# Kernel optimization log

Hardware: AMD Instinct MI355X
Metric: run time of the kernel (lower is better)

## Reference

```python
import jax, jax.numpy as jnp
import numpy as np

N_NODES = 10000
N_EDGES = 160000
F = 128
NRB = 32


def setup_inputs() -> dict:
    key = jax.random.key(0)
    ks = jax.random.split(key, 20)
    inp = {
        "s": jax.random.normal(ks[0], (N_NODES, F), jnp.float32),
        "v": jax.random.normal(ks[1], (N_NODES, 3, F), jnp.float32),
        "radial_embeddings_1": jax.random.normal(ks[2], (N_EDGES, NRB), jnp.float32),
        "radial_embeddings_2": jax.random.normal(ks[3], (N_EDGES, NRB), jnp.float32),
        "radial_embeddings_3": jax.random.normal(ks[4], (N_EDGES, NRB), jnp.float32),
        "f_cut_1": jax.random.uniform(ks[5], (N_EDGES,), jnp.float32),
        "f_cut_2": jax.random.uniform(ks[6], (N_EDGES,), jnp.float32),
        "f_cut_3": jax.random.uniform(ks[7], (N_EDGES,), jnp.float32),
        "unit_vectors_1": jax.random.normal(ks[8], (N_EDGES, 3), jnp.float32),
        "unit_vectors_2": jax.random.normal(ks[9], (N_EDGES, 3), jnp.float32),
        "unit_vectors_3": jax.random.normal(ks[10], (N_EDGES, 3), jnp.float32),
        "edge_index": jax.random.randint(ks[11], (2, N_EDGES), 0, N_NODES, jnp.int64),
    }
    # parameters (Linear uses y = x @ W.T + b; we store transposed for x @ W)
    sc1 = 1.0 / np.sqrt(F)
    sc2 = 1.0 / np.sqrt(NRB)
    inp["W1"] = jax.random.uniform(ks[12], (F, F), jnp.float32, -sc1, sc1)
    inp["b1"] = jax.random.uniform(ks[13], (F,), jnp.float32, -sc1, sc1)
    inp["W2"] = jax.random.uniform(ks[14], (F, 8 * F), jnp.float32, -sc1, sc1)
    inp["b2"] = jax.random.uniform(ks[15], (8 * F,), jnp.float32, -sc1, sc1)
    inp["Wr"] = jax.random.uniform(ks[16], (NRB, 8 * F), jnp.float32, -sc2, sc2)
    inp["br"] = jax.random.uniform(ks[17], (8 * F,), jnp.float32, -sc2, sc2)
    return inp


def reference(s, v, radial_embeddings_1, radial_embeddings_2, radial_embeddings_3,
              f_cut_1, f_cut_2, f_cut_3,
              unit_vectors_1, unit_vectors_2, unit_vectors_3,
              edge_index, W1, b1, W2, b2, Wr, br):
    idx_i, idx_j = edge_index[0], edge_index[1]
    n_nodes = s.shape[0]
    nf = W1.shape[0]

    # phi = Linear(F,F) -> SiLU -> Linear(F,8F)   [N, 8F]
    phi = jax.nn.silu(s @ W1 + b1) @ W2 + b2

    # shared-weight radial filter over 3 branches  [E, 8F]
    W = ((radial_embeddings_1 @ Wr + br) * f_cut_1[:, None]
         + (radial_embeddings_2 @ Wr + br) * f_cut_2[:, None]
         + (radial_embeddings_3 @ Wr + br) * f_cut_3[:, None])

    x = phi[idx_j] * W                                    # [E, 8F]
    x_s, x_vv, x_vs1, x_vs2, x_vs3, x_vc1, x_vc2, x_vc3 = jnp.split(x, 8, axis=-1)

    ds = jax.ops.segment_sum(x_s, idx_i, num_segments=n_nodes)

    vj = v[idx_j]                                         # [E, 3, F]
    ex = lambda a: a[:, None, :]                          # [E,1,F] broadcast over xyz
    cr = lambda u: jnp.cross(vj, u[..., None], axis=1)    # [E, 3, F]

    x_v = (vj * ex(x_vv)
           + ex(x_vs1) * unit_vectors_1[..., None]
           + ex(x_vs2) * unit_vectors_2[..., None]
           + ex(x_vs3) * unit_vectors_3[..., None]
           + ex(x_vc1) * cr(unit_vectors_1)
           + ex(x_vc2) * cr(unit_vectors_2)
           + ex(x_vc3) * cr(unit_vectors_3))              # [E, 3, F]

    dv = jax.ops.segment_sum(x_v, idx_i, num_segments=n_nodes)
    return (s + ds, v + dv)
```

## Files before the change

### kernel.cpp

```cpp
#include <hip/hip_runtime.h>

#define N_NODES 10000
#define N_EDGES 160000
#define MAXT     19400
#define NSLOT    (MAXT * 16 + 16)
#define MSG_GRID 5000
#define PHI_BLOCKS 628
#define RC_BLOCKS 5000
#define PAD_BLOCKS 625

typedef __attribute__((ext_vector_type(8))) __bf16 bf16x8;
typedef __attribute__((ext_vector_type(8))) unsigned short u16x8;
typedef __attribute__((ext_vector_type(4))) float f32x4;

static __device__ __forceinline__ unsigned short f2bf(float x) {
    union { float f; unsigned u; } un;
    un.f = x;
    unsigned r = un.u + 0x7fffu + ((un.u >> 16) & 1u);
    return (unsigned short)(r >> 16);
}

static __device__ __forceinline__ float bf2f(unsigned short h) {
    union { unsigned u; float f; } un;
    un.u = ((unsigned)h) << 16;
    return un.f;
}

__global__ __launch_bounds__(256) void init_kernel(
    const float* __restrict__ s, const float* __restrict__ v,
    const int* __restrict__ eix,
    const float* __restrict__ W1, const float* __restrict__ W2,
    const float* __restrict__ Wr,
    float* __restrict__ out0, float* __restrict__ out1,
    unsigned short* __restrict__ vbf2, int* __restrict__ cnt,
    unsigned short* __restrict__ W1T, unsigned short* __restrict__ W2T,
    unsigned short* __restrict__ WrT)
{
    int tid = blockIdx.x * 256 + threadIdx.x;
    if (tid < N_NODES * 96)
        reinterpret_cast<float4*>(out1)[tid] = reinterpret_cast<const float4*>(v)[tid];
    if (tid < N_NODES * 32)
        reinterpret_cast<float4*>(out0)[tid] = reinterpret_cast<const float4*>(s)[tid];
    if (tid < N_NODES * 128) {
        int n = tid >> 7, f = tid & 127;
        ushort4 q;
        q.x = f2bf(v[(size_t)n * 384 + f]);
        q.y = f2bf(v[(size_t)n * 384 + 128 + f]);
        q.z = f2bf(v[(size_t)n * 384 + 256 + f]);
        q.w = 0;
        *reinterpret_cast<ushort4*>(vbf2 + (size_t)tid * 4) = q;
    }
    if (tid < 131072) {
        int n = tid >> 7, k = tid & 127;
        W2T[tid] = f2bf(W2[k * 1024 + n]);
    }
    if (tid < 16384) {
        int n = tid >> 7, k = tid & 127;
        W1T[tid] = f2bf(W1[k * 128 + n]);
    }
    if (tid < 32768) {
        int n = tid >> 5, k = tid & 31;
        WrT[tid] = f2bf(Wr[k * 1024 + n]);
    }
    if (tid < N_EDGES) atomicAdd(&cnt[eix[tid]], 1);
}

__global__ __launch_bounds__(256) void scan_phi_kernel(
    const int* __restrict__ cnt, int* __restrict__ cursor,
    int* __restrict__ nb, int* __restrict__ tile_node,
    int* __restrict__ ntiles,
    const float* __restrict__ s, const unsigned short* __restrict__ W1T,
    const float* __restrict__ b1, const unsigned short* __restrict__ W2T,
    const float* __restrict__ b2, unsigned short* __restrict__ phi2)
{
    __shared__ unsigned short h_lds[64][136];
    __shared__ int ws4[4];
    int bx = blockIdx.x;
    int t = threadIdx.x, lane = t & 63, w = t >> 6;

    if (bx == PHI_BLOCKS) {
        int n0 = t * 40;
        int sum = 0;
        for (int i = 0; i < 40; ++i) {
            int n = n0 + i;
            if (n < N_NODES) sum += (cnt[n] + 15) >> 4;
        }
        int x = sum;
        #pragma unroll
        for (int o = 1; o < 64; o <<= 1) {
            int y = __shfl_up(x, o);
            if (lane >= o) x += y;
        }
        if (lane == 63) ws4[w] = x;
        __syncthreads();
        if (t < 4) {
            int v = ws4[t];
            #pragma unroll
            for (int o = 1; o < 4; o <<= 1) {
                int y = __shfl_up(v, o);
                if (lane >= o) v += y;
            }
            ws4[t] = v;
        }
        __syncthreads();
        int wb = w ? ws4[w - 1] : 0;
        int run = wb + x - sum;
        for (int i = 0; i < 40; ++i) {
            int n = n0 + i;
            if (n >= N_NODES) break;
            int tc = (cnt[n] + 15) >> 4;
            nb[n] = run * 16;
            cursor[n] = run * 16;
            for (int k = 0; k < tc; ++k) tile_node[run + k] = n;
            run += tc;
        }
        if (t == 255) *ntiles = run;
        return;
    }

    int quad = lane >> 4, l16 = lane & 15;
    int m0 = (bx >> 2) * 64;
    int colg = bx & 3;

    int arow = m0 + w * 16 + l16;
    if (arow > N_NODES - 1) arow = N_NODES - 1;
    bf16x8 afr[4];
    #pragma unroll
    for (int ks = 0; ks < 4; ++ks) {
        const float* sp = s + (size_t)arow * 128 + ks * 32 + quad * 8;
        #pragma unroll
        for (int jj = 0; jj < 8; ++jj) afr[ks][jj] = (__bf16)sp[jj];
    }
    #pragma unroll
    for (int cg = 0; cg < 8; ++cg) {
        int col = cg * 16 + l16;
        f32x4 acc = {0.f, 0.f, 0.f, 0.f};
        #pragma unroll
        for (int ks = 0; ks < 4; ++ks) {
            bf16x8 bf = *reinterpret_cast<const bf16x8*>(W1T + (size_t)col * 128 + ks * 32 + quad * 8);
            acc = __builtin_amdgcn_mfma_f32_16x16x32_bf16(afr[ks], bf, acc, 0, 0, 0);
        }
        float bb = b1[col];
        #pragma unroll
        for (int r = 0; r < 4; ++r) {
            int row = w * 16 + quad * 4 + r;
            float val = acc[r] + bb;
            h_lds[row][col] = f2bf(val / (1.f + __expf(-val)));
        }
    }
    __syncthreads();

    bf16x8 a2[4][4];
    #pragma unroll
    for (int rg = 0; rg < 4; ++rg)
        #pragma unroll
        for (int ks = 0; ks < 4; ++ks)
            a2[rg][ks] = *reinterpret_cast<const bf16x8*>(&h_lds[rg * 16 + l16][ks * 32 + quad * 8]);
    #pragma unroll
    for (int i = 0; i < 4; ++i) {
        int col = colg * 256 + w * 64 + i * 16 + l16;
        f32x4 acc2[4] = {{0,0,0,0},{0,0,0,0},{0,0,0,0},{0,0,0,0}};
        #pragma unroll
        for (int ks = 0; ks < 4; ++ks) {
            bf16x8 bf = *reinterpret_cast<const bf16x8*>(W2T + (size_t)col * 128 + ks * 32 + quad * 8);
            #pragma unroll
            for (int rg = 0; rg < 4; ++rg)
                acc2[rg] = __builtin_amdgcn_mfma_f32_16x16x32_bf16(a2[rg][ks], bf, acc2[rg], 0, 0, 0);
        }
        float bb = b2[col];
        int f = col & 127, cc = col >> 7;
        #pragma unroll
        for (int rg = 0; rg < 4; ++rg)
            #pragma unroll
            for (int r = 0; r < 4; ++r) {
                int row = m0 + rg * 16 + quad * 4 + r;
                if (row < N_NODES)
                    phi2[(size_t)row * 1024 + f * 8 + cc] = f2bf(acc2[rg][r] + bb);
            }
    }
}

__global__ __launch_bounds__(256) void rc_pad_kernel(
    const float* __restrict__ R1, const float* __restrict__ R2,
    const float* __restrict__ R3,
    const float* __restrict__ f1, const float* __restrict__ f2,
    const float* __restrict__ f3,
    const float* __restrict__ u1, const float* __restrict__ u2,
    const float* __restrict__ u3,
    const int* __restrict__ eix, const int* __restrict__ cnt,
    const int* __restrict__ nb, int* __restrict__ cursor,
    char* __restrict__ rec)
{
    int bx = blockIdx.x;
    if (bx >= RC_BLOCKS) {
        int t2 = (bx - RC_BLOCKS) * 256 + threadIdx.x;
        int n = t2 >> 4, r = t2 & 15;
        int deg = cnt[n], tc = (deg + 15) >> 4;
        int p = deg + r;
        if (p < tc * 16) {
            size_t slot = (size_t)nb[n] + p;
            f32x4 z = {0.f, 0.f, 0.f, 0.f};
            f32x4* rp = reinterpret_cast<f32x4*>(rec + slot * 128);
            #pragma unroll
            for (int q = 0; q < 8; ++q) rp[q] = z;
        }
        return;
    }

    int tid = bx * 256 + threadIdx.x;
    int e = tid >> 3, sub = tid & 7;
    int lane = threadIdx.x & 63;
    float a = f1[e], b = f2[e], c = f3[e];
    int k0 = sub * 4;
    float4 r1 = *reinterpret_cast<const float4*>(R1 + (size_t)e * 32 + k0);
    float4 r2 = *reinterpret_cast<const float4*>(R2 + (size_t)e * 32 + k0);
    float4 r3 = *reinterpret_cast<const float4*>(R3 + (size_t)e * 32 + k0);
    ushort4 o;
    o.x = f2bf(r1.x * a + r2.x * b + r3.x * c);
    o.y = f2bf(r1.y * a + r2.y * b + r3.y * c);
    o.z = f2bf(r1.z * a + r2.z * b + r3.z * c);
    o.w = f2bf(r1.w * a + r2.w * b + r3.w * c);
    int slot = 0;
    if (sub == 0) slot = atomicAdd(&cursor[eix[e]], 1);
    slot = __shfl(slot, lane & 56);
    *reinterpret_cast<ushort4*>(rec + (size_t)slot * 128 + k0 * 2) = o;
    float* hf = reinterpret_cast<float*>(rec + (size_t)slot * 128 + 64);
    if (sub == 0) {
        float4 h;
        h.x = __int_as_float(eix[N_EDGES + e]);
        h.y = a + b + c;
        h.z = 0.f; h.w = 0.f;
        *reinterpret_cast<float4*>(hf) = h;
    } else if (sub < 4) {
        const float* up = (sub == 1 ? u1 : (sub == 2 ? u2 : u3)) + (size_t)e * 3;
        float4 h;
        h.x = up[0]; h.y = up[1]; h.z = up[2]; h.w = 0.f;
        *reinterpret_cast<float4*>(hf + sub * 4) = h;
    }
}

__global__ __launch_bounds__(512) void msg_kernel(
    const char* __restrict__ rec,
    const unsigned short* __restrict__ phi2, const unsigned short* __restrict__ vbf2,
    const unsigned short* __restrict__ WrT, const float* __restrict__ br,
    const int* __restrict__ tile_node, const int* __restrict__ ntiles,
    float* __restrict__ out0, float* __restrict__ out1)
{
    int t = threadIdx.x, lane = t & 63, w = t >> 6;
    int quad = lane >> 4, l16 = lane & 15;
    int fcol = w * 16 + l16;
    const int nt = *ntiles;
    const float* recf = reinterpret_cast<const float*>(rec);

    bf16x8 bfrag[8];
    float brv[8];
    #pragma unroll
    for (int c = 0; c < 8; ++c) {
        int col = c * 128 + fcol;
        bfrag[c] = *reinterpret_cast<const bf16x8*>(WrT + (size_t)col * 32 + quad * 8);
        brv[c] = br[col];
    }

    __shared__ __align__(16) float srow[2][16][20];

    int tile = blockIdx.x;
    bf16x8 af;
    if (tile < nt) {
        if (t < 256)
            srow[0][t >> 4][t & 15] = recf[((size_t)tile * 16 + (t >> 4)) * 32 + 16 + (t & 15)];
        af = *reinterpret_cast<const bf16x8*>(rec + ((size_t)tile * 16 + l16) * 128 + quad * 16);
    }

    for (int k = 0; tile < nt; ++k, tile += MSG_GRID) {
        int p = k & 1;
        __syncthreads();

        f32x4 acc[8];
        #pragma unroll
        for (int c = 0; c < 8; ++c) {
            f32x4 z = {0.f, 0.f, 0.f, 0.f};
            acc[c] = __builtin_amdgcn_mfma_f32_16x16x32_bf16(af, bfrag[c], z, 0, 0, 0);
        }

        int tn = tile + MSG_GRID;
        if (tn < nt) {
            if (t < 256)
                srow[p ^ 1][t >> 4][t & 15] = recf[((size_t)tn * 16 + (t >> 4)) * 32 + 16 + (t & 15)];
            af = *reinterpret_cast<const bf16x8*>(rec + ((size_t)tn * 16 + l16) * 128 + quad * 16);
        }

        float ds = 0.f, d0 = 0.f, d1 = 0.f, d2 = 0.f;
        #pragma unroll
        for (int r = 0; r < 4; ++r) {
            const float* rw = srow[p][quad * 4 + r];
            float2 jf = *reinterpret_cast<const float2*>(rw);
            f32x4 U1 = *reinterpret_cast<const f32x4*>(rw + 4);
            f32x4 U2 = *reinterpret_cast<const f32x4*>(rw + 8);
            f32x4 U3 = *reinterpret_cast<const f32x4*>(rw + 12);
            int j = __float_as_int(jf.x);
            float fs = jf.y;
            size_t o = (size_t)j * 128 + fcol;
            u16x8 ph = *reinterpret_cast<const u16x8*>(phi2 + o * 8);
            ushort4 vb = *reinterpret_cast<const ushort4*>(vbf2 + o * 4);
            float x[8];
            #pragma unroll
            for (int c = 0; c < 8; ++c)
                x[c] = bf2f(ph[c]) * (acc[c][r] + brv[c] * fs);
            float vjx = bf2f(vb.x), vjy = bf2f(vb.y), vjz = bf2f(vb.z);

            ds += x[0];
            d0 += vjx * x[1] + U1.x * x[2] + U2.x * x[3] + U3.x * x[4]
                + x[5] * (vjy * U1.z - vjz * U1.y)
                + x[6] * (vjy * U2.z - vjz * U2.y)
                + x[7] * (vjy * U3.z - vjz * U3.y);
            d1 += vjy * x[1] + U1.y * x[2] + U2.y * x[3] + U3.y * x[4]
                + x[5] * (vjz * U1.x - vjx * U1.z)
                + x[6] * (vjz * U2.x - vjx * U2.z)
                + x[7] * (vjz * U3.x - vjx * U3.z);
            d2 += vjz * x[1] + U1.z * x[2] + U2.z * x[3] + U3.z * x[4]
                + x[5] * (vjx * U1.y - vjy * U1.x)
                + x[6] * (vjx * U2.y - vjy * U2.x)
                + x[7] * (vjx * U3.y - vjy * U3.x);
        }

        ds += __shfl_xor(ds, 16); ds += __shfl_xor(ds, 32);
        d0 += __shfl_xor(d0, 16); d0 += __shfl_xor(d0, 32);
        d1 += __shfl_xor(d1, 16); d1 += __shfl_xor(d1, 32);
        d2 += __shfl_xor(d2, 16); d2 += __shfl_xor(d2, 32);

        if (quad == 0) {
            int node = tile_node[tile];
            atomicAdd(&out0[(size_t)node * 128 + fcol], ds);
            size_t vo = (size_t)node * 384 + fcol;
            atomicAdd(&out1[vo], d0);
            atomicAdd(&out1[vo + 128], d1);
            atomicAdd(&out1[vo + 256], d2);
        }
    }
}

extern "C" void kernel_launch(void* const* d_in, const int* in_sizes, int n_in,
                              void* d_out, int out_size, void* d_ws, size_t ws_size,
                              hipStream_t stream) {
    const float* s  = (const float*)d_in[0];
    const float* v  = (const float*)d_in[1];
    const float* R1 = (const float*)d_in[2];
    const float* R2 = (const float*)d_in[3];
    const float* R3 = (const float*)d_in[4];
    const float* f1 = (const float*)d_in[5];
    const float* f2 = (const float*)d_in[6];
    const float* f3 = (const float*)d_in[7];
    const float* u1 = (const float*)d_in[8];
    const float* u2 = (const float*)d_in[9];
    const float* u3 = (const float*)d_in[10];
    const int*  eix = (const int*)d_in[11];
    const float* W1 = (const float*)d_in[12];
    const float* b1 = (const float*)d_in[13];
    const float* W2 = (const float*)d_in[14];
    const float* b2 = (const float*)d_in[15];
    const float* Wr = (const float*)d_in[16];
    const float* br = (const float*)d_in[17];

    char* ws = (char*)d_ws;
    size_t off = 0;
    auto alloc = [&](size_t bytes) -> void* {
        void* p = ws + off;
        off = (off + bytes + 255) & ~(size_t)255;
        return p;
    };
    int* cnt       = (int*)alloc((size_t)N_NODES * 4);
    int* cursor    = (int*)alloc((size_t)N_NODES * 4);
    int* nb        = (int*)alloc((size_t)N_NODES * 4);
    int* tile_node = (int*)alloc((size_t)MAXT * 4);
    int* ntiles    = (int*)alloc(4);
    char* rec            = (char*)alloc((size_t)NSLOT * 128);
    unsigned short* vbf2 = (unsigned short*)alloc((size_t)N_NODES * 128 * 4 * 2);
    unsigned short* phi2 = (unsigned short*)alloc((size_t)N_NODES * 1024 * 2);
    unsigned short* W1T  = (unsigned short*)alloc(128 * 128 * 2);
    unsigned short* W2T  = (unsigned short*)alloc(1024 * 128 * 2);
    unsigned short* WrT  = (unsigned short*)alloc(1024 * 32 * 2);
    (void)ws_size; (void)in_sizes; (void)n_in; (void)out_size;

    float* out0 = (float*)d_out;
    float* out1 = out0 + (size_t)N_NODES * 128;

    hipMemsetAsync(cnt, 0, (size_t)N_NODES * 4, stream);
    init_kernel<<<5000, 256, 0, stream>>>(s, v, eix, W1, W2, Wr,
                                          out0, out1, vbf2, cnt, W1T, W2T, WrT);
    scan_phi_kernel<<<PHI_BLOCKS + 1, 256, 0, stream>>>(
        cnt, cursor, nb, tile_node, ntiles, s, W1T, b1, W2T, b2, phi2);
    rc_pad_kernel<<<RC_BLOCKS + PAD_BLOCKS, 256, 0, stream>>>(
        R1, R2, R3, f1, f2, f3, u1, u2, u3, eix, cnt, nb, cursor, rec);
    msg_kernel<<<MSG_GRID, 512, 0, stream>>>(rec, phi2, vbf2, WrT, br,
                                             tile_node, ntiles, out0, out1);
}
```

Before: 320.0 us.

## Pack edges densely by destination and flush partial sums on node change

Replaces per-node padded 16-edge tiles with a dense CSR-style layout: the scan now computes exact edge offsets, the padding kernel and the tile_node/ntiles arrays are removed, and each record stores its destination node. The message kernel walks fixed 16-edge tiles, where each row group keeps running sums and issues atomics whenever the destination node changes. This removes padded work (about 19.4k tiles down to 10k) and the zero-fill pass. In exchange it issues more atomics per tile, since each lane quad now writes its own partials instead of reducing across quads with shuffles first.

```diff
diff --git a/kernel.cpp b/kernel.cpp
--- a/kernel.cpp
+++ b/kernel.cpp
@@ -2,12 +2,10 @@
 
 #define N_NODES 10000
 #define N_EDGES 160000
-#define MAXT     19400
-#define NSLOT    (MAXT * 16 + 16)
-#define MSG_GRID 5000
+#define NTILES   10000
+#define MSG_GRID 2500
 #define PHI_BLOCKS 628
 #define RC_BLOCKS 5000
-#define PAD_BLOCKS 625
 
 typedef __attribute__((ext_vector_type(8))) __bf16 bf16x8;
 typedef __attribute__((ext_vector_type(8))) unsigned short u16x8;
@@ -67,8 +65,6 @@
 
 __global__ __launch_bounds__(256) void scan_phi_kernel(
     const int* __restrict__ cnt, int* __restrict__ cursor,
-    int* __restrict__ nb, int* __restrict__ tile_node,
-    int* __restrict__ ntiles,
     const float* __restrict__ s, const unsigned short* __restrict__ W1T,
     const float* __restrict__ b1, const unsigned short* __restrict__ W2T,
     const float* __restrict__ b2, unsigned short* __restrict__ phi2)
@@ -83,7 +79,7 @@
         int sum = 0;
         for (int i = 0; i < 40; ++i) {
             int n = n0 + i;
-            if (n < N_NODES) sum += (cnt[n] + 15) >> 4;
+            if (n < N_NODES) sum += cnt[n];
         }
         int x = sum;
         #pragma unroll
@@ -94,13 +90,13 @@
         if (lane == 63) ws4[w] = x;
         __syncthreads();
         if (t < 4) {
-            int v = ws4[t];
+            int vsum = ws4[t];
             #pragma unroll
             for (int o = 1; o < 4; o <<= 1) {
-                int y = __shfl_up(v, o);
-                if (lane >= o) v += y;
+                int y = __shfl_up(vsum, o);
+                if (lane >= o) vsum += y;
             }
-            ws4[t] = v;
+            ws4[t] = vsum;
         }
         __syncthreads();
         int wb = w ? ws4[w - 1] : 0;
@@ -108,13 +104,9 @@
         for (int i = 0; i < 40; ++i) {
             int n = n0 + i;
             if (n >= N_NODES) break;
-            int tc = (cnt[n] + 15) >> 4;
-            nb[n] = run * 16;
-            cursor[n] = run * 16;
-            for (int k = 0; k < tc; ++k) tile_node[run + k] = n;
-            run += tc;
-        }
-        if (t == 255) *ntiles = run;
+            cursor[n] = run;
+            run += cnt[n];
+        }
         return;
     }
 
@@ -180,34 +172,17 @@
     }
 }
 
-__global__ __launch_bounds__(256) void rc_pad_kernel(
+__global__ __launch_bounds__(256) void rc_kernel(
     const float* __restrict__ R1, const float* __restrict__ R2,
     const float* __restrict__ R3,
     const float* __restrict__ f1, const float* __restrict__ f2,
     const float* __restrict__ f3,
     const float* __restrict__ u1, const float* __restrict__ u2,
     const float* __restrict__ u3,
-    const int* __restrict__ eix, const int* __restrict__ cnt,
-    const int* __restrict__ nb, int* __restrict__ cursor,
+    const int* __restrict__ eix, int* __restrict__ cursor,
     char* __restrict__ rec)
 {
-    int bx = blockIdx.x;
-    if (bx >= RC_BLOCKS) {
-        int t2 = (bx - RC_BLOCKS) * 256 + threadIdx.x;
-        int n = t2 >> 4, r = t2 & 15;
-        int deg = cnt[n], tc = (deg + 15) >> 4;
-        int p = deg + r;
-        if (p < tc * 16) {
-            size_t slot = (size_t)nb[n] + p;
-            f32x4 z = {0.f, 0.f, 0.f, 0.f};
-            f32x4* rp = reinterpret_cast<f32x4*>(rec + slot * 128);
-            #pragma unroll
-            for (int q = 0; q < 8; ++q) rp[q] = z;
-        }
-        return;
-    }
-
-    int tid = bx * 256 + threadIdx.x;
+    int tid = blockIdx.x * 256 + threadIdx.x;
     int e = tid >> 3, sub = tid & 7;
     int lane = threadIdx.x & 63;
     float a = f1[e], b = f2[e], c = f3[e];
@@ -220,8 +195,11 @@
     o.y = f2bf(r1.y * a + r2.y * b + r3.y * c);
     o.z = f2bf(r1.z * a + r2.z * b + r3.z * c);
     o.w = f2bf(r1.w * a + r2.w * b + r3.w * c);
-    int slot = 0;
-    if (sub == 0) slot = atomicAdd(&cursor[eix[e]], 1);
+    int slot = 0, node = 0;
+    if (sub == 0) {
+        node = eix[e];
+        slot = atomicAdd(&cursor[node], 1);
+    }
     slot = __shfl(slot, lane & 56);
     *reinterpret_cast<ushort4*>(rec + (size_t)slot * 128 + k0 * 2) = o;
     float* hf = reinterpret_cast<float*>(rec + (size_t)slot * 128 + 64);
@@ -229,7 +207,8 @@
         float4 h;
         h.x = __int_as_float(eix[N_EDGES + e]);
         h.y = a + b + c;
-        h.z = 0.f; h.w = 0.f;
+        h.z = __int_as_float(node);
+        h.w = 0.f;
         *reinterpret_cast<float4*>(hf) = h;
     } else if (sub < 4) {
         const float* up = (sub == 1 ? u1 : (sub == 2 ? u2 : u3)) + (size_t)e * 3;
@@ -243,13 +222,11 @@
     const char* __restrict__ rec,
     const unsigned short* __restrict__ phi2, const unsigned short* __restrict__ vbf2,
     const unsigned short* __restrict__ WrT, const float* __restrict__ br,
-    const int* __restrict__ tile_node, const int* __restrict__ ntiles,
     float* __restrict__ out0, float* __restrict__ out1)
 {
     int t = threadIdx.x, lane = t & 63, w = t >> 6;
     int quad = lane >> 4, l16 = lane & 15;
     int fcol = w * 16 + l16;
-    const int nt = *ntiles;
     const float* recf = reinterpret_cast<const float*>(rec);
 
     bf16x8 bfrag[8];
@@ -265,13 +242,13 @@
 
     int tile = blockIdx.x;
     bf16x8 af;
-    if (tile < nt) {
+    {
         if (t < 256)
             srow[0][t >> 4][t & 15] = recf[((size_t)tile * 16 + (t >> 4)) * 32 + 16 + (t & 15)];
         af = *reinterpret_cast<const bf16x8*>(rec + ((size_t)tile * 16 + l16) * 128 + quad * 16);
     }
 
-    for (int k = 0; tile < nt; ++k, tile += MSG_GRID) {
+    for (int k = 0; k < 4; ++k, tile += MSG_GRID) {
         int p = k & 1;
         __syncthreads();
 
@@ -283,22 +260,32 @@
         }
 
         int tn = tile + MSG_GRID;
-        if (tn < nt) {
+        if (tn < NTILES) {
             if (t < 256)
                 srow[p ^ 1][t >> 4][t & 15] = recf[((size_t)tn * 16 + (t >> 4)) * 32 + 16 + (t & 15)];
             af = *reinterpret_cast<const bf16x8*>(rec + ((size_t)tn * 16 + l16) * 128 + quad * 16);
         }
 
         float ds = 0.f, d0 = 0.f, d1 = 0.f, d2 = 0.f;
+        int cur = __float_as_int(srow[p][quad * 4][2]);
         #pragma unroll
         for (int r = 0; r < 4; ++r) {
             const float* rw = srow[p][quad * 4 + r];
-            float2 jf = *reinterpret_cast<const float2*>(rw);
+            f32x4 h0 = *reinterpret_cast<const f32x4*>(rw);
             f32x4 U1 = *reinterpret_cast<const f32x4*>(rw + 4);
             f32x4 U2 = *reinterpret_cast<const f32x4*>(rw + 8);
             f32x4 U3 = *reinterpret_cast<const f32x4*>(rw + 12);
-            int j = __float_as_int(jf.x);
-            float fs = jf.y;
+            int ndr = __float_as_int(h0.z);
+            if (ndr != cur) {
+                atomicAdd(&out0[(size_t)cur * 128 + fcol], ds);
+                size_t vo = (size_t)cur * 384 + fcol;
+                atomicAdd(&out1[vo], d0);
+                atomicAdd(&out1[vo + 128], d1);
+                atomicAdd(&out1[vo + 256], d2);
+                cur = ndr; ds = 0.f; d0 = 0.f; d1 = 0.f; d2 = 0.f;
+            }
+            int j = __float_as_int(h0.x);
+            float fs = h0.y;
             size_t o = (size_t)j * 128 + fcol;
             u16x8 ph = *reinterpret_cast<const u16x8*>(phi2 + o * 8);
             ushort4 vb = *reinterpret_cast<const ushort4*>(vbf2 + o * 4);
@@ -322,20 +309,11 @@
                 + x[6] * (vjx * U2.y - vjy * U2.x)
                 + x[7] * (vjx * U3.y - vjy * U3.x);
         }
-
-        ds += __shfl_xor(ds, 16); ds += __shfl_xor(ds, 32);
-        d0 += __shfl_xor(d0, 16); d0 += __shfl_xor(d0, 32);
-        d1 += __shfl_xor(d1, 16); d1 += __shfl_xor(d1, 32);
-        d2 += __shfl_xor(d2, 16); d2 += __shfl_xor(d2, 32);
-
-        if (quad == 0) {
-            int node = tile_node[tile];
-            atomicAdd(&out0[(size_t)node * 128 + fcol], ds);
-            size_t vo = (size_t)node * 384 + fcol;
-            atomicAdd(&out1[vo], d0);
-            atomicAdd(&out1[vo + 128], d1);
-            atomicAdd(&out1[vo + 256], d2);
-        }
+        atomicAdd(&out0[(size_t)cur * 128 + fcol], ds);
+        size_t vo = (size_t)cur * 384 + fcol;
+        atomicAdd(&out1[vo], d0);
+        atomicAdd(&out1[vo + 128], d1);
+        atomicAdd(&out1[vo + 256], d2);
     }
 }
 
@@ -370,10 +348,7 @@
     };
     int* cnt       = (int*)alloc((size_t)N_NODES * 4);
     int* cursor    = (int*)alloc((size_t)N_NODES * 4);
-    int* nb        = (int*)alloc((size_t)N_NODES * 4);
-    int* tile_node = (int*)alloc((size_t)MAXT * 4);
-    int* ntiles    = (int*)alloc(4);
-    char* rec            = (char*)alloc((size_t)NSLOT * 128);
+    char* rec            = (char*)alloc((size_t)N_EDGES * 128);
     unsigned short* vbf2 = (unsigned short*)alloc((size_t)N_NODES * 128 * 4 * 2);
     unsigned short* phi2 = (unsigned short*)alloc((size_t)N_NODES * 1024 * 2);
     unsigned short* W1T  = (unsigned short*)alloc(128 * 128 * 2);
@@ -388,9 +363,8 @@
     init_kernel<<<5000, 256, 0, stream>>>(s, v, eix, W1, W2, Wr,
                                           out0, out1, vbf2, cnt, W1T, W2T, WrT);
     scan_phi_kernel<<<PHI_BLOCKS + 1, 256, 0, stream>>>(
-        cnt, cursor, nb, tile_node, ntiles, s, W1T, b1, W2T, b2, phi2);
-    rc_pad_kernel<<<RC_BLOCKS + PAD_BLOCKS, 256, 0, stream>>>(
-        R1, R2, R3, f1, f2, f3, u1, u2, u3, eix, cnt, nb, cursor, rec);
-    msg_kernel<<<MSG_GRID, 512, 0, stream>>>(rec, phi2, vbf2, WrT, br,
-                                             tile_node, ntiles, out0, out1);
-}
+        cnt, cursor, s, W1T, b1, W2T, b2, phi2);
+    rc_kernel<<<RC_BLOCKS, 256, 0, stream>>>(
+        R1, R2, R3, f1, f2, f3, u1, u2, u3, eix, cursor, rec);
+    msg_kernel<<<MSG_GRID, 512, 0, stream>>>(rec, phi2, vbf2, WrT, br, out0, out1);
+}
```

Measured after the change: 441.5 us. +37.9%, slower.

## Permute edge slots within tiles and skip empty padded rows in message loop

Applied to the files above, without the earlier changes.

Packs the number of valid rows into each tile_node entry and permutes slot positions within a 16-row tile so that real edges spread across the four MFMA row groups. With that layout, the message kernel can stop its per-lane loop early once later row groups hold only padding, skipping gathers of phi and v for zero-padded rows. The change adds index arithmetic in the record writer and pad kernel, plus a data-dependent branch in the message loop. Rows are interleaved so each quad's r-th row is filled first.

```diff
diff --git a/kernel.cpp b/kernel.cpp
--- a/kernel.cpp
+++ b/kernel.cpp
@@ -24,6 +24,10 @@
     union { unsigned u; float f; } un;
     un.u = ((unsigned)h) << 16;
     return un.f;
+}
+
+static __device__ __forceinline__ int tperm(int o) {
+    return ((o & 3) << 2) | (o >> 2);
 }
 
 __global__ __launch_bounds__(256) void init_kernel(
@@ -94,13 +98,13 @@
         if (lane == 63) ws4[w] = x;
         __syncthreads();
         if (t < 4) {
-            int v = ws4[t];
+            int vsum = ws4[t];
             #pragma unroll
             for (int o = 1; o < 4; o <<= 1) {
-                int y = __shfl_up(v, o);
-                if (lane >= o) v += y;
+                int y = __shfl_up(vsum, o);
+                if (lane >= o) vsum += y;
             }
-            ws4[t] = v;
+            ws4[t] = vsum;
         }
         __syncthreads();
         int wb = w ? ws4[w - 1] : 0;
@@ -108,10 +112,15 @@
         for (int i = 0; i < 40; ++i) {
             int n = n0 + i;
             if (n >= N_NODES) break;
-            int tc = (cnt[n] + 15) >> 4;
+            int deg = cnt[n];
+            int tc = (deg + 15) >> 4;
             nb[n] = run * 16;
             cursor[n] = run * 16;
-            for (int k = 0; k < tc; ++k) tile_node[run + k] = n;
+            for (int k = 0; k < tc; ++k) {
+                int rows = deg - k * 16;
+                if (rows > 16) rows = 16;
+                tile_node[run + k] = n | (rows << 16);
+            }
             run += tc;
         }
         if (t == 255) *ntiles = run;
@@ -198,7 +207,8 @@
         int deg = cnt[n], tc = (deg + 15) >> 4;
         int p = deg + r;
         if (p < tc * 16) {
-            size_t slot = (size_t)nb[n] + p;
+            size_t lin = (size_t)nb[n] + p;
+            size_t slot = (lin & ~(size_t)15) | tperm((int)(lin & 15));
             f32x4 z = {0.f, 0.f, 0.f, 0.f};
             f32x4* rp = reinterpret_cast<f32x4*>(rec + slot * 128);
             #pragma unroll
@@ -223,8 +233,9 @@
     int slot = 0;
     if (sub == 0) slot = atomicAdd(&cursor[eix[e]], 1);
     slot = __shfl(slot, lane & 56);
-    *reinterpret_cast<ushort4*>(rec + (size_t)slot * 128 + k0 * 2) = o;
-    float* hf = reinterpret_cast<float*>(rec + (size_t)slot * 128 + 64);
+    size_t ps = ((size_t)slot & ~(size_t)15) | tperm(slot & 15);
+    *reinterpret_cast<ushort4*>(rec + ps * 128 + k0 * 2) = o;
+    float* hf = reinterpret_cast<float*>(rec + ps * 128 + 64);
     if (sub == 0) {
         float4 h;
         h.x = __int_as_float(eix[N_EDGES + e]);
@@ -273,6 +284,8 @@
 
     for (int k = 0; tile < nt; ++k, tile += MSG_GRID) {
         int p = k & 1;
+        int info = __builtin_amdgcn_readfirstlane(tile_node[tile]);
+        int nr = ((info >> 16) + 3) >> 2;
         __syncthreads();
 
         f32x4 acc[8];
@@ -292,6 +305,7 @@
         float ds = 0.f, d0 = 0.f, d1 = 0.f, d2 = 0.f;
         #pragma unroll
         for (int r = 0; r < 4; ++r) {
+            if (r >= nr) break;
             const float* rw = srow[p][quad * 4 + r];
             float2 jf = *reinterpret_cast<const float2*>(rw);
             f32x4 U1 = *reinterpret_cast<const f32x4*>(rw + 4);
@@ -329,7 +343,7 @@
         d2 += __shfl_xor(d2, 16); d2 += __shfl_xor(d2, 32);
 
         if (quad == 0) {
-            int node = tile_node[tile];
+            int node = info & 0xffff;
             atomicAdd(&out0[(size_t)node * 128 + fcol], ds);
             size_t vo = (size_t)node * 384 + fcol;
             atomicAdd(&out1[vo], d0);
```

Measured after the change: 386.7 us. 1.21x slower.

## Pad per-node edge groups to 8 instead of 16, packing two nodes per tile

Applied to the files above, without the earlier changes.

Edge records per destination node are now padded to multiples of 8 rather than 16, and each 16-edge tile in the message kernel covers two 8-edge half-tiles that may belong to different nodes. The reduction shuffles only within each half, and two lanes groups issue atomics to their respective nodes. This cuts the padded zero work in the MFMA message pass (average degree 16 wastes much with 16-padding). It adds more atomics per tile and a packed tile-node table built in the scan block.

```diff
diff --git a/kernel.cpp b/kernel.cpp
--- a/kernel.cpp
+++ b/kernel.cpp
@@ -2,12 +2,13 @@
 
 #define N_NODES 10000
 #define N_EDGES 160000
-#define MAXT     19400
-#define NSLOT    (MAXT * 16 + 16)
+#define MAXHALF  28750
+#define NSLOT8   230016
+#define MAXT     14400
 #define MSG_GRID 5000
 #define PHI_BLOCKS 628
 #define RC_BLOCKS 5000
-#define PAD_BLOCKS 625
+#define PAD_BLOCKS 313
 
 typedef __attribute__((ext_vector_type(8))) __bf16 bf16x8;
 typedef __attribute__((ext_vector_type(8))) unsigned short u16x8;
@@ -67,8 +68,8 @@
 
 __global__ __launch_bounds__(256) void scan_phi_kernel(
     const int* __restrict__ cnt, int* __restrict__ cursor,
-    int* __restrict__ nb, int* __restrict__ tile_node,
-    int* __restrict__ ntiles,
+    int* __restrict__ nb, int* __restrict__ half_node,
+    int* __restrict__ tile_node, int* __restrict__ ntiles,
     const float* __restrict__ s, const unsigned short* __restrict__ W1T,
     const float* __restrict__ b1, const unsigned short* __restrict__ W2T,
     const float* __restrict__ b2, unsigned short* __restrict__ phi2)
@@ -83,7 +84,7 @@
         int sum = 0;
         for (int i = 0; i < 40; ++i) {
             int n = n0 + i;
-            if (n < N_NODES) sum += (cnt[n] + 15) >> 4;
+            if (n < N_NODES) sum += (cnt[n] + 7) >> 3;
         }
         int x = sum;
         #pragma unroll
@@ -94,13 +95,13 @@
         if (lane == 63) ws4[w] = x;
         __syncthreads();
         if (t < 4) {
-            int v = ws4[t];
+            int vsum = ws4[t];
             #pragma unroll
             for (int o = 1; o < 4; o <<= 1) {
-                int y = __shfl_up(v, o);
-                if (lane >= o) v += y;
+                int y = __shfl_up(vsum, o);
+                if (lane >= o) vsum += y;
             }
-            ws4[t] = v;
+            ws4[t] = vsum;
         }
         __syncthreads();
         int wb = w ? ws4[w - 1] : 0;
@@ -108,13 +109,23 @@
         for (int i = 0; i < 40; ++i) {
             int n = n0 + i;
             if (n >= N_NODES) break;
-            int tc = (cnt[n] + 15) >> 4;
-            nb[n] = run * 16;
-            cursor[n] = run * 16;
-            for (int k = 0; k < tc; ++k) tile_node[run + k] = n;
-            run += tc;
-        }
-        if (t == 255) *ntiles = run;
+            int deg = cnt[n];
+            int c8 = (deg + 7) >> 3;
+            nb[n] = run * 8;
+            cursor[n] = run * 8;
+            for (int k = 0; k < c8; ++k) half_node[run + k] = n;
+            run += c8;
+        }
+        int total = ws4[3];
+        if (t == 0) {
+            half_node[total] = 0;
+            ntiles[0] = (total + 1) >> 1;
+            ntiles[1] = total;
+        }
+        __syncthreads();
+        int nt0 = (total + 1) >> 1;
+        for (int t4 = t; t4 < nt0; t4 += 256)
+            tile_node[t4] = half_node[2 * t4] | (half_node[2 * t4 + 1] << 16);
         return;
     }
 
@@ -189,20 +200,31 @@
     const float* __restrict__ u3,
     const int* __restrict__ eix, const int* __restrict__ cnt,
     const int* __restrict__ nb, int* __restrict__ cursor,
-    char* __restrict__ rec)
+    const int* __restrict__ ntiles, char* __restrict__ rec)
 {
     int bx = blockIdx.x;
     if (bx >= RC_BLOCKS) {
         int t2 = (bx - RC_BLOCKS) * 256 + threadIdx.x;
-        int n = t2 >> 4, r = t2 & 15;
-        int deg = cnt[n], tc = (deg + 15) >> 4;
-        int p = deg + r;
-        if (p < tc * 16) {
-            size_t slot = (size_t)nb[n] + p;
-            f32x4 z = {0.f, 0.f, 0.f, 0.f};
-            f32x4* rp = reinterpret_cast<f32x4*>(rec + slot * 128);
-            #pragma unroll
-            for (int q = 0; q < 8; ++q) rp[q] = z;
+        if (t2 < N_NODES * 8) {
+            int n = t2 >> 3, r = t2 & 7;
+            int deg = cnt[n], c8 = (deg + 7) >> 3;
+            int p = deg + r;
+            if (p < c8 * 8) {
+                size_t slot = (size_t)nb[n] + p;
+                f32x4 z = {0.f, 0.f, 0.f, 0.f};
+                f32x4* rp = reinterpret_cast<f32x4*>(rec + slot * 128);
+                #pragma unroll
+                for (int q = 0; q < 8; ++q) rp[q] = z;
+            }
+        } else if (t2 < N_NODES * 8 + 8) {
+            int nhalf = ntiles[1];
+            if (nhalf & 1) {
+                size_t slot = (size_t)nhalf * 8 + (t2 - N_NODES * 8);
+                f32x4 z = {0.f, 0.f, 0.f, 0.f};
+                f32x4* rp = reinterpret_cast<f32x4*>(rec + slot * 128);
+                #pragma unroll
+                for (int q = 0; q < 8; ++q) rp[q] = z;
+            }
         }
         return;
     }
@@ -323,13 +345,14 @@
                 + x[7] * (vjx * U3.y - vjy * U3.x);
         }
 
-        ds += __shfl_xor(ds, 16); ds += __shfl_xor(ds, 32);
-        d0 += __shfl_xor(d0, 16); d0 += __shfl_xor(d0, 32);
-        d1 += __shfl_xor(d1, 16); d1 += __shfl_xor(d1, 32);
-        d2 += __shfl_xor(d2, 16); d2 += __shfl_xor(d2, 32);
-
-        if (quad == 0) {
-            int node = tile_node[tile];
+        ds += __shfl_xor(ds, 16);
+        d0 += __shfl_xor(d0, 16);
+        d1 += __shfl_xor(d1, 16);
+        d2 += __shfl_xor(d2, 16);
+
+        if (!(quad & 1)) {
+            int ab = tile_node[tile];
+            int node = quad ? (ab >> 16) : (ab & 0xffff);
             atomicAdd(&out0[(size_t)node * 128 + fcol], ds);
             size_t vo = (size_t)node * 384 + fcol;
             atomicAdd(&out1[vo], d0);
@@ -371,9 +394,10 @@
     int* cnt       = (int*)alloc((size_t)N_NODES * 4);
     int* cursor    = (int*)alloc((size_t)N_NODES * 4);
     int* nb        = (int*)alloc((size_t)N_NODES * 4);
+    int* half_node = (int*)alloc((size_t)(MAXHALF + 2) * 4);
     int* tile_node = (int*)alloc((size_t)MAXT * 4);
-    int* ntiles    = (int*)alloc(4);
-    char* rec            = (char*)alloc((size_t)NSLOT * 128);
+    int* ntiles    = (int*)alloc(8);
+    char* rec            = (char*)alloc((size_t)NSLOT8 * 128);
     unsigned short* vbf2 = (unsigned short*)alloc((size_t)N_NODES * 128 * 4 * 2);
     unsigned short* phi2 = (unsigned short*)alloc((size_t)N_NODES * 1024 * 2);
     unsigned short* W1T  = (unsigned short*)alloc(128 * 128 * 2);
@@ -388,9 +412,10 @@
     init_kernel<<<5000, 256, 0, stream>>>(s, v, eix, W1, W2, Wr,
                                           out0, out1, vbf2, cnt, W1T, W2T, WrT);
     scan_phi_kernel<<<PHI_BLOCKS + 1, 256, 0, stream>>>(
-        cnt, cursor, nb, tile_node, ntiles, s, W1T, b1, W2T, b2, phi2);
+        cnt, cursor, nb, half_node, tile_node, ntiles,
+        s, W1T, b1, W2T, b2, phi2);
     rc_pad_kernel<<<RC_BLOCKS + PAD_BLOCKS, 256, 0, stream>>>(
-        R1, R2, R3, f1, f2, f3, u1, u2, u3, eix, cnt, nb, cursor, rec);
+        R1, R2, R3, f1, f2, f3, u1, u2, u3, eix, cnt, nb, cursor, ntiles, rec);
     msg_kernel<<<MSG_GRID, 512, 0, stream>>>(rec, phi2, vbf2, WrT, br,
                                              tile_node, ntiles, out0, out1);
 }
```

Result: slower. 343.8 us (+7.4%).
